# Performance work log

Measured on AMD Instinct MI355X. Metric: run time of the kernel, lower is better.

Reference implementation:

```python
import jax, jax.numpy as jnp
import numpy as np

BS, C1, NY, NX = 8, 64, 256, 256
C2, K, P = 64, 3, 1
N = 131072  # number of active (b, y, x) indices


def setup_inputs() -> dict:
    key = jax.random.key(0)
    k1, k2, k3, k4, k5, k6 = jax.random.split(key, 6)
    x = jax.random.normal(k1, (BS, C1, NY, NX), dtype=jnp.float32)
    bi = jax.random.randint(k2, (N,), 0, BS)
    yi = jax.random.randint(k3, (N,), 0, NY)
    xi = jax.random.randint(k4, (N,), 0, NX)
    indices = jnp.stack([bi, yi, xi], axis=1).astype(jnp.int32)
    weight = jax.random.normal(k5, (C2, C1, K, K), dtype=jnp.float32) * 0.05
    bias = jax.random.normal(k6, (C2,), dtype=jnp.float32) * 0.05
    return {"x": x, "indices": indices, "weight": weight, "bias": bias}


def reference(x, indices, weight, bias):
    # x: [bs, c1, ny, nx]; indices: [N, 3] of (b, y, x); weight: [c2, c1, k, k]
    bs, c1, ny, nx = x.shape
    c2, _, k, _ = weight.shape
    p = (k - 1) // 2  # asserted k == 2p + 1 in original
    xp = jnp.pad(x, ((0, 0), (0, 0), (p, p), (p, p)))  # zero-pad like F.unfold
    bi, yi, xi = indices[:, 0], indices[:, 1], indices[:, 2]
    dy = jnp.arange(k)
    dx = jnp.arange(k)
    rows = yi[:, None, None] + dy[None, :, None]  # [N, k, 1]
    cols = xi[:, None, None] + dx[None, None, :]  # [N, 1, k]
    # gather only active patches (equiv. to unfold[bi, yi, xi] in the original)
    # advanced indices at dims 0,2,3 -> result [N, k, k, c1]
    patches = xp[bi[:, None, None], :, rows, cols]
    # F.unfold channel ordering is (c1, kh, kw) flattened
    patches = patches.transpose(0, 3, 1, 2).reshape(patches.shape[0], c1 * k * k)
    w_flat = weight.reshape(c2, c1 * k * k)
    z = patches @ w_flat.T + bias  # [N, c2]
    return z
```

## Files before the change

kernel.cpp:

```cpp
#include <hip/hip_runtime.h>
#include <hip/hip_bf16.h>
#include <stdint.h>

#define NPTS 131072

typedef __attribute__((ext_vector_type(8))) short bf16x8;
typedef __attribute__((ext_vector_type(4))) float f32x4;
typedef __attribute__((ext_vector_type(8))) unsigned short u16x8;

__device__ inline unsigned short f32_to_bf16(float f) {
    union { float f; uint32_t u; } v; v.f = f;
    uint32_t u = v.u;
    return (unsigned short)((u + 0x7FFFu + ((u >> 16) & 1u)) >> 16);
}

__global__ __launch_bounds__(256) void k_transpose(const float* __restrict__ x,
                                                   unsigned short* __restrict__ xt) {
    __shared__ float tile[64][65];
    int bid = blockIdx.x;
    int batch = bid >> 10;
    int pix0 = (bid & 1023) << 6;
    int t = threadIdx.x;
    const float* xb = x + (size_t)batch * 64 * 65536;

    int c0 = t >> 4;
    int px = (t & 15) << 2;
#pragma unroll
    for (int i = 0; i < 4; ++i) {
        int c = c0 + i * 16;
        float4 v = *(const float4*)(xb + (size_t)c * 65536 + pix0 + px);
        tile[c][px + 0] = v.x; tile[c][px + 1] = v.y;
        tile[c][px + 2] = v.z; tile[c][px + 3] = v.w;
    }
    __syncthreads();

    int c8 = (t & 7) << 3;
    int pp = t >> 3;
#pragma unroll
    for (int h = 0; h < 2; ++h) {
        int pix = pp + h * 32;
        u16x8 o;
#pragma unroll
        for (int i = 0; i < 8; ++i) o[i] = f32_to_bf16(tile[c8 + i][pix]);
        *(u16x8*)(xt + ((size_t)(batch * 65536 + pix0 + pix) * 64 + c8)) = o;
    }
}

__global__ __launch_bounds__(256) void k_wreorder(const float* __restrict__ w,
                                                  unsigned short* __restrict__ wtn) {
    int o = blockIdx.x * 256 + threadIdx.x;
    if (o >= 64 * 576) return;
    int c2 = o / 576;
    int rem = o - c2 * 576;
    int q = rem >> 6;
    int c = rem & 63;
    wtn[o] = f32_to_bf16(w[c2 * 576 + c * 9 + q]);
}

__global__ __launch_bounds__(512, 4) void k_gather_gemm(
    const unsigned short* __restrict__ xt,
    const unsigned short* __restrict__ wtn,
    const int* __restrict__ indices,
    const float* __restrict__ bias,
    float* __restrict__ out) {
    __shared__ unsigned short wlds[64 * 584];

    int t = threadIdx.x;
    int tile = blockIdx.x;
    int w = t >> 6;
    int l = t & 63;
    int lo = l & 15;
    int hi = l >> 4;

#pragma unroll
    for (int i = 0; i < 9; ++i) {
        int m = t + i * 512;
        int row = m / 72;
        int col = (m - row * 72) * 8;
        *(u16x8*)(&wlds[row * 584 + col]) = *(const u16x8*)(wtn + row * 576 + col);
    }

    int pt = tile * 128 + w * 16 + lo;
    int b  = indices[pt * 3 + 0];
    int yi = indices[pt * 3 + 1];
    int xi = indices[pt * 3 + 2];

    uint32_t off[9];
    bool val[9];
#pragma unroll
    for (int q = 0; q < 9; ++q) {
        int yy = yi + (q / 3) - 1;
        int xx = xi + (q % 3) - 1;
        bool v = ((unsigned)yy < 256u) & ((unsigned)xx < 256u);
        uint32_t pix = ((uint32_t)b << 16) + ((uint32_t)(yy & 255) << 8) + (uint32_t)(xx & 255);
        val[q] = v;
        off[q] = (v ? pix * 128u : 0u) + (uint32_t)(hi << 4);
    }

    auto lda = [&](int q, int half) -> bf16x8 {
        const u16x8* p = (const u16x8*)((const char*)xt + off[q] + half * 64);
        u16x8 d = *p;
        u16x8 z = {};
        return (bf16x8)(val[q] ? d : z);
    };

    f32x4 acc[4];
#pragma unroll
    for (int nn = 0; nn < 4; ++nn) acc[nn] = (f32x4)0.0f;

    __syncthreads();

    bf16x8 a0 = lda(0, 0), a1 = lda(0, 1);
#pragma unroll
    for (int q = 0; q < 9; ++q) {
        bf16x8 n0, n1;
        if (q < 8) { n0 = lda(q + 1, 0); n1 = lda(q + 1, 1); }
#pragma unroll
        for (int nn = 0; nn < 4; ++nn) {
            bf16x8 b0 = *(const bf16x8*)(&wlds[(nn * 16 + lo) * 584 + q * 64 + (hi << 3)]);
            acc[nn] = __builtin_amdgcn_mfma_f32_16x16x32_bf16(a0, b0, acc[nn], 0, 0, 0);
        }
#pragma unroll
        for (int nn = 0; nn < 4; ++nn) {
            bf16x8 b1 = *(const bf16x8*)(&wlds[(nn * 16 + lo) * 584 + q * 64 + 32 + (hi << 3)]);
            acc[nn] = __builtin_amdgcn_mfma_f32_16x16x32_bf16(a1, b1, acc[nn], 0, 0, 0);
        }
        a0 = n0; a1 = n1;
    }

    int row_base = tile * 128 + w * 16 + (hi << 2);
#pragma unroll
    for (int nn = 0; nn < 4; ++nn) {
        float bv = bias[nn * 16 + lo];
#pragma unroll
        for (int r = 0; r < 4; ++r) {
            out[(size_t)(row_base + r) * 64 + nn * 16 + lo] = acc[nn][r] + bv;
        }
        (void)bv;
    }
}

__global__ void k_naive(const float* __restrict__ x, const int* __restrict__ idx,
                        const float* __restrict__ w, const float* __restrict__ bias,
                        float* __restrict__ out) {
    int i = blockIdx.x * 256 + threadIdx.x;
    if (i >= NPTS * 64) return;
    int p = i >> 6, c2 = i & 63;
    int b = idx[p * 3], yi = idx[p * 3 + 1], xi = idx[p * 3 + 2];
    float acc = bias[c2];
    for (int c = 0; c < 64; ++c) {
        const float* xp = x + ((size_t)(b * 64 + c) << 16);
        const float* wp = w + (c2 * 64 + c) * 9;
        for (int dy = 0; dy < 3; ++dy) {
            int yy = yi + dy - 1;
            if ((unsigned)yy >= 256u) continue;
            for (int dx = 0; dx < 3; ++dx) {
                int xx = xi + dx - 1;
                if ((unsigned)xx >= 256u) continue;
                acc += xp[(yy << 8) + xx] * wp[dy * 3 + dx];
            }
        }
    }
    out[i] = acc;
}

extern "C" void kernel_launch(void* const* d_in, const int* in_sizes, int n_in,
                              void* d_out, int out_size, void* d_ws, size_t ws_size,
                              hipStream_t stream) {
    const float* x       = (const float*)d_in[0];
    const int*   indices = (const int*)d_in[1];
    const float* weight  = (const float*)d_in[2];
    const float* bias    = (const float*)d_in[3];
    float* out = (float*)d_out;

    size_t xt_bytes = (size_t)8 * 65536 * 64 * 2;
    size_t need = xt_bytes + (size_t)64 * 576 * 2;
    if (ws_size < need) {
        k_naive<<<(NPTS * 64 + 255) / 256, 256, 0, stream>>>(x, indices, weight, bias, out);
        return;
    }
    unsigned short* xt  = (unsigned short*)d_ws;
    unsigned short* wtn = (unsigned short*)((char*)d_ws + xt_bytes);

    k_transpose<<<8192, 256, 0, stream>>>(x, xt);
    k_wreorder<<<(64 * 576 + 255) / 256, 256, 0, stream>>>(weight, wtn);
    k_gather_gemm<<<NPTS / 128, 512, 0, stream>>>(xt, wtn, indices, bias, out);
}
```

Measured before the change: 67.17 us.

## Fuse weight reorder into transpose, prefragment weights, double points per wave

```diff
diff --git a/kernel.cpp b/kernel.cpp
--- a/kernel.cpp
+++ b/kernel.cpp
@@ -15,7 +15,32 @@
 }
 
 __global__ __launch_bounds__(256) void k_transpose(const float* __restrict__ x,
-                                                   unsigned short* __restrict__ xt) {
+                                                   unsigned short* __restrict__ xt,
+                                                   const float* __restrict__ w,
+                                                   unsigned short* __restrict__ wfrag) {
+    if (blockIdx.x >= 8192) {
+        int tid = (blockIdx.x - 8192) * 256 + threadIdx.x;
+        if (tid < 4608) {
+            int ci = tid >> 6;
+            int l  = tid & 63;
+            int q    = ci >> 3;
+            int half = (ci >> 2) & 1;
+            int nn   = ci & 3;
+            int c2   = nn * 16 + (l & 15);
+            int cin0 = half * 32 + ((l >> 4) << 3);
+            u16x8 o;
+#pragma unroll
+            for (int e = 0; e < 8; ++e)
+                o[e] = f32_to_bf16(w[c2 * 576 + (cin0 + e) * 9 + q]);
+            *(u16x8*)(wfrag + tid * 8) = o;
+        }
+        if (blockIdx.x == 8192 && threadIdx.x < 8) {
+            u16x8 z = {};
+            *(u16x8*)(xt + (size_t)8 * 65536 * 64 + threadIdx.x * 8) = z;
+        }
+        return;
+    }
+
     __shared__ float tile[64][65];
     int bid = blockIdx.x;
     int batch = bid >> 10;
@@ -46,27 +71,15 @@
     }
 }
 
-__global__ __launch_bounds__(256) void k_wreorder(const float* __restrict__ w,
-                                                  unsigned short* __restrict__ wtn) {
-    int o = blockIdx.x * 256 + threadIdx.x;
-    if (o >= 64 * 576) return;
-    int c2 = o / 576;
-    int rem = o - c2 * 576;
-    int q = rem >> 6;
-    int c = rem & 63;
-    wtn[o] = f32_to_bf16(w[c2 * 576 + c * 9 + q]);
-}
-
 __global__ __launch_bounds__(512, 4) void k_gather_gemm(
     const unsigned short* __restrict__ xt,
-    const unsigned short* __restrict__ wtn,
+    const unsigned short* __restrict__ wfrag,
     const int* __restrict__ indices,
     const float* __restrict__ bias,
     float* __restrict__ out) {
-    __shared__ unsigned short wlds[64 * 584];
+    __shared__ unsigned short wlds[72 * 512];
 
     int t = threadIdx.x;
-    int tile = blockIdx.x;
     int w = t >> 6;
     int l = t & 63;
     int lo = l & 15;
@@ -75,68 +88,75 @@
 #pragma unroll
     for (int i = 0; i < 9; ++i) {
         int m = t + i * 512;
-        int row = m / 72;
-        int col = (m - row * 72) * 8;
-        *(u16x8*)(&wlds[row * 584 + col]) = *(const u16x8*)(wtn + row * 576 + col);
-    }
-
-    int pt = tile * 128 + w * 16 + lo;
-    int b  = indices[pt * 3 + 0];
-    int yi = indices[pt * 3 + 1];
-    int xi = indices[pt * 3 + 2];
-
-    uint32_t off[9];
-    bool val[9];
-#pragma unroll
-    for (int q = 0; q < 9; ++q) {
-        int yy = yi + (q / 3) - 1;
-        int xx = xi + (q % 3) - 1;
+        *(u16x8*)(&wlds[m * 8]) = *(const u16x8*)(wfrag + m * 8);
+    }
+
+    int p0 = blockIdx.x * 256 + w * 32;
+    int pA = p0 + lo, pB = p0 + 16 + lo;
+    int bA = indices[pA * 3], yA = indices[pA * 3 + 1], xA = indices[pA * 3 + 2];
+    int bB = indices[pB * 3], yB = indices[pB * 3 + 1], xB = indices[pB * 3 + 2];
+
+    const uint32_t PADOFF = (uint32_t)8 * 65536 * 128;
+    uint32_t sub = (uint32_t)(hi << 4);
+
+    auto offq = [&](int b, int y, int x, int q) -> uint32_t {
+        int yy = y + (q / 3) - 1;
+        int xx = x + (q % 3) - 1;
         bool v = ((unsigned)yy < 256u) & ((unsigned)xx < 256u);
         uint32_t pix = ((uint32_t)b << 16) + ((uint32_t)(yy & 255) << 8) + (uint32_t)(xx & 255);
-        val[q] = v;
-        off[q] = (v ? pix * 128u : 0u) + (uint32_t)(hi << 4);
-    }
-
-    auto lda = [&](int q, int half) -> bf16x8 {
-        const u16x8* p = (const u16x8*)((const char*)xt + off[q] + half * 64);
-        u16x8 d = *p;
-        u16x8 z = {};
-        return (bf16x8)(val[q] ? d : z);
+        return (v ? pix * 128u : PADOFF) + sub;
     };
-
-    f32x4 acc[4];
-#pragma unroll
-    for (int nn = 0; nn < 4; ++nn) acc[nn] = (f32x4)0.0f;
+    auto lda = [&](uint32_t o) -> bf16x8 {
+        return (bf16x8)(*(const u16x8*)((const char*)xt + o));
+    };
+
+    f32x4 acc[2][4];
+#pragma unroll
+    for (int m = 0; m < 2; ++m)
+#pragma unroll
+        for (int nn = 0; nn < 4; ++nn) acc[m][nn] = (f32x4)0.0f;
 
     __syncthreads();
 
-    bf16x8 a0 = lda(0, 0), a1 = lda(0, 1);
+    uint32_t oA = offq(bA, yA, xA, 0), oB = offq(bB, yB, xB, 0);
+    bf16x8 a00 = lda(oA), a01 = lda(oA + 64);
+    bf16x8 a10 = lda(oB), a11 = lda(oB + 64);
+
 #pragma unroll
     for (int q = 0; q < 9; ++q) {
-        bf16x8 n0, n1;
-        if (q < 8) { n0 = lda(q + 1, 0); n1 = lda(q + 1, 1); }
+        bf16x8 n00, n01, n10, n11;
+        if (q < 8) {
+            uint32_t nA = offq(bA, yA, xA, q + 1), nB = offq(bB, yB, xB, q + 1);
+            n00 = lda(nA); n01 = lda(nA + 64);
+            n10 = lda(nB); n11 = lda(nB + 64);
+        }
+        const unsigned short* base = &wlds[q * 4096];
 #pragma unroll
         for (int nn = 0; nn < 4; ++nn) {
-            bf16x8 b0 = *(const bf16x8*)(&wlds[(nn * 16 + lo) * 584 + q * 64 + (hi << 3)]);
-            acc[nn] = __builtin_amdgcn_mfma_f32_16x16x32_bf16(a0, b0, acc[nn], 0, 0, 0);
+            bf16x8 b0 = *(const bf16x8*)(base + nn * 512 + l * 8);
+            acc[0][nn] = __builtin_amdgcn_mfma_f32_16x16x32_bf16(a00, b0, acc[0][nn], 0, 0, 0);
+            acc[1][nn] = __builtin_amdgcn_mfma_f32_16x16x32_bf16(a10, b0, acc[1][nn], 0, 0, 0);
         }
 #pragma unroll
         for (int nn = 0; nn < 4; ++nn) {
-            bf16x8 b1 = *(const bf16x8*)(&wlds[(nn * 16 + lo) * 584 + q * 64 + 32 + (hi << 3)]);
-            acc[nn] = __builtin_amdgcn_mfma_f32_16x16x32_bf16(a1, b1, acc[nn], 0, 0, 0);
-        }
-        a0 = n0; a1 = n1;
-    }
-
-    int row_base = tile * 128 + w * 16 + (hi << 2);
+            bf16x8 b1 = *(const bf16x8*)(base + 2048 + nn * 512 + l * 8);
+            acc[0][nn] = __builtin_amdgcn_mfma_f32_16x16x32_bf16(a01, b1, acc[0][nn], 0, 0, 0);
+            acc[1][nn] = __builtin_amdgcn_mfma_f32_16x16x32_bf16(a11, b1, acc[1][nn], 0, 0, 0);
+        }
+        if (q < 8) { a00 = n00; a01 = n01; a10 = n10; a11 = n11; }
+    }
+
+    int rbase = blockIdx.x * 256 + w * 32 + (hi << 2);
 #pragma unroll
     for (int nn = 0; nn < 4; ++nn) {
         float bv = bias[nn * 16 + lo];
 #pragma unroll
-        for (int r = 0; r < 4; ++r) {
-            out[(size_t)(row_base + r) * 64 + nn * 16 + lo] = acc[nn][r] + bv;
-        }
-        (void)bv;
+        for (int m = 0; m < 2; ++m) {
+#pragma unroll
+            for (int r = 0; r < 4; ++r) {
+                out[(size_t)(rbase + m * 16 + r) * 64 + nn * 16 + lo] = acc[m][nn][r] + bv;
+            }
+        }
     }
 }
 
@@ -173,16 +193,15 @@
     const float* bias    = (const float*)d_in[3];
     float* out = (float*)d_out;
 
-    size_t xt_bytes = (size_t)8 * 65536 * 64 * 2;
-    size_t need = xt_bytes + (size_t)64 * 576 * 2;
+    size_t xt_bytes = (size_t)8 * 65536 * 64 * 2 + 128;
+    size_t need = xt_bytes + (size_t)72 * 1024;
     if (ws_size < need) {
         k_naive<<<(NPTS * 64 + 255) / 256, 256, 0, stream>>>(x, indices, weight, bias, out);
         return;
     }
-    unsigned short* xt  = (unsigned short*)d_ws;
-    unsigned short* wtn = (unsigned short*)((char*)d_ws + xt_bytes);
-
-    k_transpose<<<8192, 256, 0, stream>>>(x, xt);
-    k_wreorder<<<(64 * 576 + 255) / 256, 256, 0, stream>>>(weight, wtn);
-    k_gather_gemm<<<NPTS / 128, 512, 0, stream>>>(xt, wtn, indices, bias, out);
-}
+    unsigned short* xt    = (unsigned short*)d_ws;
+    unsigned short* wfrag = (unsigned short*)((char*)d_ws + xt_bytes);
+
+    k_transpose<<<8192 + 18, 256, 0, stream>>>(x, xt, weight, wfrag);
+    k_gather_gemm<<<NPTS / 256, 512, 0, stream>>>(xt, wfrag, indices, bias, out);
+}
```

New measurement: 63.92 us (median of 2 runs). 4.8% less time.
